# Performance work log

Hardware: AMD Instinct MI355X
Metric: run time of the kernel (lower is better)

Reference implementation:

```python
import jax, jax.numpy as jnp
import numpy as np

N_NODES = 100000
N_EDGES = 1600000
MSG = 16
HID = 16
N_ETYPE = 8
N_CLASSES = 40


def setup_inputs() -> dict:
    key = jax.random.key(0)
    ks = jax.random.split(key, 11)
    return {
        "features": jax.random.normal(ks[0], (N_NODES, HID), dtype=jnp.float32),
        "src": jax.random.randint(ks[1], (N_EDGES,), 0, N_NODES),
        "dst": jax.random.randint(ks[2], (N_EDGES,), 0, N_NODES),
        "etype": jax.random.randint(ks[3], (N_EDGES,), 0, N_ETYPE),
        "edge_matrix": jax.random.normal(ks[4], (N_ETYPE, MSG * HID), dtype=jnp.float32) * 0.1,
        "w_ih": jax.random.normal(ks[5], (3 * HID, MSG), dtype=jnp.float32) * 0.1,
        "w_hh": jax.random.normal(ks[6], (3 * HID, HID), dtype=jnp.float32) * 0.1,
        "b_ih": jax.random.normal(ks[7], (3 * HID,), dtype=jnp.float32) * 0.1,
        "b_hh": jax.random.normal(ks[8], (3 * HID,), dtype=jnp.float32) * 0.1,
        "out_w": jax.random.normal(ks[9], (N_CLASSES, HID), dtype=jnp.float32) * 0.1,
        "out_b": jax.random.normal(ks[10], (N_CLASSES,), dtype=jnp.float32) * 0.1,
    }


def reference(features, src, dst, etype, edge_matrix, w_ih, w_hh, b_ih, b_hh, out_w, out_b):
    n = features.shape[0]
    # message: per-edge [MSG,HID] matrix (gathered by edge type) times src h
    A = edge_matrix[etype].reshape(-1, MSG, HID)          # [E, MSG, HID]
    msg = jnp.einsum('emh,eh->em', A, features[src])      # [E, MSG]
    # reduce: scatter-sum messages onto destination nodes
    m = jax.ops.segment_sum(msg, dst, num_segments=n)     # [N, MSG]
    # apply: one GRU step per node (PyTorch nn.GRU gate math)
    gi = m @ w_ih.T + b_ih                                # [N, 3*HID]
    gh = features @ w_hh.T + b_hh                         # [N, 3*HID]
    i_r, i_z, i_n = jnp.split(gi, 3, axis=-1)
    h_r, h_z, h_n = jnp.split(gh, 3, axis=-1)
    r = jax.nn.sigmoid(i_r + h_r)
    z = jax.nn.sigmoid(i_z + h_z)
    c = jnp.tanh(i_n + r * h_n)
    h = (1.0 - z) * c + z * features                      # [N, HID]
    return h @ out_w.T + out_b                            # [N, N_CLASSES]
```

## Files before the change

### kernel.cpp

```cpp
#include <hip/hip_runtime.h>
#include <math.h>

constexpr int N_NODES   = 100000;
constexpr int N_EDGES   = 1600000;
constexpr int MSG       = 16;
constexpr int HID       = 16;
constexpr int N_ETYPE   = 8;
constexpr int N_CLASSES = 40;

constexpr int CBSIZE   = 256;
constexpr int NBUCKET  = (N_NODES + CBSIZE - 1) / CBSIZE;
constexpr int SBSIZE   = 32;
constexpr int NSUB     = 8;
constexpr int NSB      = NBUCKET * NSUB;
constexpr int EPB      = 4096;
constexpr int NEBLK    = (N_EDGES + EPB - 1) / EPB;
constexpr int REC_CAP  = 5120;
constexpr int FGRID    = 1536;
constexpr int NSLOT    = 2048;
constexpr int A_STRIDE = 260;
constexpr int SRECC    = 1792;

__device__ __forceinline__ float sigmoidf_(float x) { return 1.0f / (1.0f + __expf(-x)); }
__device__ __forceinline__ float tanhf_(float x) { float e = __expf(2.0f * x); return 1.0f - 2.0f / (e + 1.0f); }

__device__ __forceinline__ unsigned f2bf(float f) {
    unsigned u = __float_as_uint(f);
    return (u + 0x7FFFu + ((u >> 16) & 1u)) >> 16;
}
__device__ __forceinline__ float bflo(unsigned u) { return __uint_as_float(u << 16); }
__device__ __forceinline__ float bfhi(unsigned u) { return __uint_as_float(u & 0xFFFF0000u); }

__global__ void __launch_bounds__(256) cvt_kernel(const float* __restrict__ features,
                                                  uint4* __restrict__ featb,
                                                  int* __restrict__ gcursor) {
    int i = blockIdx.x * 256 + threadIdx.x;
    if (i < NBUCKET) gcursor[i] = i * REC_CAP;
    if (i * 8 >= N_NODES * HID) return;
    const float4* fp = reinterpret_cast<const float4*>(features + i * 8);
    float4 a = fp[0], b = fp[1];
    uint4 o;
    o.x = f2bf(a.x) | (f2bf(a.y) << 16);
    o.y = f2bf(a.z) | (f2bf(a.w) << 16);
    o.z = f2bf(b.x) | (f2bf(b.y) << 16);
    o.w = f2bf(b.z) | (f2bf(b.w) << 16);
    featb[i] = o;
}

__global__ void __launch_bounds__(512) partition_kernel(
    const int* __restrict__ src,
    const int* __restrict__ dst,
    const int* __restrict__ etype,
    int* __restrict__ gcursor,
    int* __restrict__ records)
{
    __shared__ int srec[EPB];
    __shared__ unsigned short sbkt[EPB];
    __shared__ int lh[NBUCKET];
    __shared__ int lscan[NBUCKET];
    __shared__ int gbarr[NBUCKET];
    __shared__ int wsum[8];

    int t = threadIdx.x;
    int base = blockIdx.x * EPB;

    for (int i = t; i < NBUCKET; i += 512) lh[i] = 0;
    __syncthreads();

    int rr[8]; int bb[8]; int rk[8];
    #pragma unroll
    for (int q = 0; q < 8; ++q) {
        int e = base + t + 512 * q;
        if (e < N_EDGES) {
            int d = dst[e];
            bb[q] = d >> 8;
            rr[q] = (src[e] << 11) | (etype[e] << 8) | (d & 255);
            rk[q] = atomicAdd(&lh[bb[q]], 1);
        } else bb[q] = -1;
    }
    __syncthreads();

    int i0 = t * 4;
    int v0 = 0, v1 = 0, v2 = 0, v3 = 0;
    if (i0     < NBUCKET) v0 = lh[i0];
    if (i0 + 1 < NBUCKET) v1 = lh[i0 + 1];
    if (i0 + 2 < NBUCKET) v2 = lh[i0 + 2];
    if (i0 + 3 < NBUCKET) v3 = lh[i0 + 3];
    int tsum = v0 + v1 + v2 + v3;

    int lane = t & 63, w = t >> 6;
    int inc = tsum;
    #pragma unroll
    for (int off = 1; off < 64; off <<= 1) {
        int u = __shfl_up(inc, off, 64);
        if (lane >= off) inc += u;
    }
    if (lane == 63) wsum[w] = inc;
    __syncthreads();
    int basew = 0;
    #pragma unroll
    for (int i = 0; i < 8; ++i) if (i < w) basew += wsum[i];
    int excl = basew + inc - tsum;

    if (i0     < NBUCKET) { lscan[i0]     = excl; gbarr[i0]     = v0 ? atomicAdd(&gcursor[i0],     v0) : 0; } excl += v0;
    if (i0 + 1 < NBUCKET) { lscan[i0 + 1] = excl; gbarr[i0 + 1] = v1 ? atomicAdd(&gcursor[i0 + 1], v1) : 0; } excl += v1;
    if (i0 + 2 < NBUCKET) { lscan[i0 + 2] = excl; gbarr[i0 + 2] = v2 ? atomicAdd(&gcursor[i0 + 2], v2) : 0; } excl += v2;
    if (i0 + 3 < NBUCKET) { lscan[i0 + 3] = excl; gbarr[i0 + 3] = v3 ? atomicAdd(&gcursor[i0 + 3], v3) : 0; }
    __syncthreads();

    #pragma unroll
    for (int q = 0; q < 8; ++q) {
        if (bb[q] >= 0) {
            int sidx = lscan[bb[q]] + rk[q];
            srec[sidx] = rr[q];
            sbkt[sidx] = (unsigned short)bb[q];
        }
    }
    __syncthreads();

    int cnt = min(EPB, N_EDGES - base);
    for (int s2 = t; s2 < cnt; s2 += 512) {
        int b2 = sbkt[s2];
        int pos = gbarr[b2] + (s2 - lscan[b2]);
        if (pos < (b2 + 1) * REC_CAP)
            records[pos] = srec[s2];
    }
}

__global__ void __launch_bounds__(256) partition2_kernel(
    const int* __restrict__ gcursor,
    const int* __restrict__ records,
    int* __restrict__ records2,
    int* __restrict__ slot_off)
{
    __shared__ int hist[NSLOT];
    __shared__ int wsum[4];
    __shared__ int srec[REC_CAP];

    int cb = blockIdx.x;
    int beg = cb * REC_CAP;
    int cnt = min(gcursor[cb] - beg, REC_CAP);
    int t = threadIdx.x;

    #pragma unroll
    for (int j = 0; j < 8; ++j) hist[t * 8 + j] = 0;
    __syncthreads();

    for (int i = t; i < cnt; i += 256) {
        int r = records[beg + i];
        atomicAdd(&hist[((r & 255) << 3) | ((r >> 8) & 7)], 1);
    }
    __syncthreads();

    int loc[8]; int tsum = 0;
    #pragma unroll
    for (int j = 0; j < 8; ++j) { loc[j] = hist[t * 8 + j]; tsum += loc[j]; }

    int lane = t & 63, w = t >> 6;
    int inc = tsum;
    #pragma unroll
    for (int off = 1; off < 64; off <<= 1) {
        int u = __shfl_up(inc, off, 64);
        if (lane >= off) inc += u;
    }
    if (lane == 63) wsum[w] = inc;
    __syncthreads();
    int basew = 0;
    #pragma unroll
    for (int i = 0; i < 4; ++i) if (i < w) basew += wsum[i];
    int excl = basew + inc - tsum;

    #pragma unroll
    for (int j = 0; j < 8; ++j) {
        slot_off[cb * (NSLOT + 1) + t * 8 + j] = beg + excl;
        hist[t * 8 + j] = excl;
        excl += loc[j];
    }
    if (t == 0) slot_off[cb * (NSLOT + 1) + NSLOT] = beg + cnt;
    __syncthreads();

    for (int i = t; i < cnt; i += 256) {
        int r = records[beg + i];
        int pos = atomicAdd(&hist[((r & 255) << 3) | ((r >> 8) & 7)], 1);
        srec[pos] = r;
    }
    __syncthreads();
    for (int i = t; i < cnt; i += 256) records2[beg + i] = srec[i];
}

__global__ void __launch_bounds__(256, 6) fused_kernel(
    const uint4* __restrict__ featb,
    const float* __restrict__ features,
    const int*   __restrict__ slot_off,
    const int*   __restrict__ records2,
    const float* __restrict__ edge_matrix,
    const float* __restrict__ w_ih,
    const float* __restrict__ w_hh,
    const float* __restrict__ b_ih,
    const float* __restrict__ b_hh,
    const float* __restrict__ out_w,
    const float* __restrict__ out_b,
    float*       __restrict__ out)
{
    __shared__ float A[N_ETYPE * A_STRIDE];
    __shared__ float wihL[3 * HID * 17];
    __shared__ float whhL[3 * HID * 17];
    __shared__ float outwL[N_CLASSES * 17];
    __shared__ float bihL[3 * HID];
    __shared__ float bhhL[3 * HID];
    __shared__ float outbL[N_CLASSES];
    __shared__ int   srecL[SRECC];

    int t = threadIdx.x;
    int dl = t >> 3, q = t & 7;
    const float4* feat4 = reinterpret_cast<const float4*>(features);

    for (int i = t; i < N_ETYPE * MSG * HID; i += 256)
        A[(i >> 8) * A_STRIDE + (i & 255)] = edge_matrix[i];
    for (int i = t; i < 3 * HID * MSG; i += 256) wihL[(i >> 4) * 17 + (i & 15)] = w_ih[i];
    for (int i = t; i < 3 * HID * HID; i += 256) whhL[(i >> 4) * 17 + (i & 15)] = w_hh[i];
    for (int i = t; i < N_CLASSES * HID; i += 256) outwL[(i >> 4) * 17 + (i & 15)] = out_w[i];
    if (t < 48) bihL[t] = b_ih[t];
    else if (t < 96) bhhL[t - 48] = b_hh[t - 48];
    else if (t < 136) outbL[t - 96] = out_b[t - 96];

    for (int b = blockIdx.x; b < NSB; b += FGRID) {
        int nodeBase = b * SBSIZE;
        if (nodeBase >= N_NODES) continue;
        int cb = b >> 3, sb = b & 7;
        __syncthreads();

        int sobase = cb * (NSLOT + 1) + sb * 256;
        int S0 = slot_off[sobase];
        int S1 = slot_off[sobase + 256];
        int begin = slot_off[sobase + t];
        int end   = slot_off[sobase + t + 1];
        int lim = min(S1 - S0, SRECC);
        for (int i = t; i < lim; i += 256)
            srecL[i] = __builtin_nontemporal_load(records2 + S0 + i);
        __syncthreads();

        float acc[16];
        #pragma unroll
        for (int k = 0; k < 16; ++k) acc[k] = 0.0f;
        for (int i = begin; i < end; ++i) {
            int li = i - S0;
            int rec = (li < SRECC) ? srecL[li] : records2[i];
            int sn = rec >> 11;
            uint4 ua = featb[2 * sn], ub = featb[2 * sn + 1];
            acc[0]  += bflo(ua.x); acc[1]  += bfhi(ua.x);
            acc[2]  += bflo(ua.y); acc[3]  += bfhi(ua.y);
            acc[4]  += bflo(ua.z); acc[5]  += bfhi(ua.z);
            acc[6]  += bflo(ua.w); acc[7]  += bfhi(ua.w);
            acc[8]  += bflo(ub.x); acc[9]  += bfhi(ub.x);
            acc[10] += bflo(ub.y); acc[11] += bfhi(ub.y);
            acc[12] += bflo(ub.z); acc[13] += bfhi(ub.z);
            acc[14] += bflo(ub.w); acc[15] += bfhi(ub.w);
        }

        float p[16];
        {
            const float* Aq = &A[q * A_STRIDE];
            #pragma unroll
            for (int mm = 0; mm < 16; ++mm) {
                const float4* Ar = reinterpret_cast<const float4*>(Aq + mm * 16);
                float4 x0 = Ar[0], x1 = Ar[1], x2 = Ar[2], x3 = Ar[3];
                p[mm] = x0.x*acc[0]  + x0.y*acc[1]  + x0.z*acc[2]  + x0.w*acc[3]
                      + x1.x*acc[4]  + x1.y*acc[5]  + x1.z*acc[6]  + x1.w*acc[7]
                      + x2.x*acc[8]  + x2.y*acc[9]  + x2.z*acc[10] + x2.w*acc[11]
                      + x3.x*acc[12] + x3.y*acc[13] + x3.z*acc[14] + x3.w*acc[15];
            }
        }
        #pragma unroll
        for (int mm = 0; mm < 16; ++mm) {
            p[mm] += __shfl_xor(p[mm], 1, 64);
            p[mm] += __shfl_xor(p[mm], 2, 64);
            p[mm] += __shfl_xor(p[mm], 4, 64);
        }

        int n = nodeBase + dl;
        float hva[16];
        {
            const float4* hp = feat4 + (size_t)n * 4;
            float4 h0 = hp[0], h1 = hp[1], h2 = hp[2], h3 = hp[3];
            hva[0]=h0.x; hva[1]=h0.y; hva[2]=h0.z; hva[3]=h0.w;
            hva[4]=h1.x; hva[5]=h1.y; hva[6]=h1.z; hva[7]=h1.w;
            hva[8]=h2.x; hva[9]=h2.y; hva[10]=h2.z; hva[11]=h2.w;
            hva[12]=h3.x; hva[13]=h3.y; hva[14]=h3.z; hva[15]=h3.w;
        }
        float hg[2];
        #pragma unroll
        for (int jj = 0; jj < 2; ++jj) {
            int j = 2 * q + jj;
            float ir  = bihL[j];
            float iz  = bihL[j + HID];
            float inn = bihL[j + 2 * HID];
            float hr  = bhhL[j];
            float hz  = bhhL[j + HID];
            float hnn = bhhL[j + 2 * HID];
            const float* wir = &wihL[j * 17];
            const float* wiz = &wihL[(j + HID) * 17];
            const float* win = &wihL[(j + 2 * HID) * 17];
            const float* whr = &whhL[j * 17];
            const float* whz = &whhL[(j + HID) * 17];
            const float* whn = &whhL[(j + 2 * HID) * 17];
            #pragma unroll
            for (int k = 0; k < HID; ++k) {
                ir  += wir[k] * p[k];
                iz  += wiz[k] * p[k];
                inn += win[k] * p[k];
                hr  += whr[k] * hva[k];
                hz  += whz[k] * hva[k];
                hnn += whn[k] * hva[k];
            }
            float rg = sigmoidf_(ir + hr);
            float zg = sigmoidf_(iz + hz);
            float cg = tanhf_(inn + rg * hnn);
            float hj = features[(size_t)n * HID + j];
            hg[jj] = (1.0f - zg) * cg + zg * hj;
        }

        int lanebase = (t & 63) & 56;
        float hh[16];
        #pragma unroll
        for (int qq = 0; qq < 8; ++qq) {
            hh[2 * qq]     = __shfl(hg[0], lanebase + qq, 64);
            hh[2 * qq + 1] = __shfl(hg[1], lanebase + qq, 64);
        }

        float* op = out + (size_t)n * N_CLASSES + 5 * q;
        #pragma unroll
        for (int cc = 0; cc < 5; ++cc) {
            int c = 5 * q + cc;
            float a2 = outbL[c];
            const float* wr = &outwL[c * 17];
            #pragma unroll
            for (int k = 0; k < HID; ++k) a2 += wr[k] * hh[k];
            __builtin_nontemporal_store(a2, op + cc);
        }
    }
}

extern "C" void kernel_launch(void* const* d_in, const int* in_sizes, int n_in,
                              void* d_out, int out_size, void* d_ws, size_t ws_size,
                              hipStream_t stream) {
    const float* features    = (const float*)d_in[0];
    const int*   src         = (const int*)  d_in[1];
    const int*   dst         = (const int*)  d_in[2];
    const int*   etype       = (const int*)  d_in[3];
    const float* edge_matrix = (const float*)d_in[4];
    const float* w_ih        = (const float*)d_in[5];
    const float* w_hh        = (const float*)d_in[6];
    const float* b_ih        = (const float*)d_in[7];
    const float* b_hh        = (const float*)d_in[8];
    const float* out_w       = (const float*)d_in[9];
    const float* out_b       = (const float*)d_in[10];
    float* out = (float*)d_out;

    int* gcursor  = (int*)d_ws;
    int* slot_off = gcursor + NBUCKET;
    int* records  = slot_off + NBUCKET * (NSLOT + 1);
    int* records2 = records + NBUCKET * REC_CAP;
    size_t featb_off = ((size_t)((char*)(records2 + NBUCKET * REC_CAP) - (char*)d_ws) + 15) & ~15ull;
    uint4* featb = (uint4*)((char*)d_ws + featb_off);

    cvt_kernel<<<(N_NODES * HID / 8 + 255) / 256, 256, 0, stream>>>(features, featb, gcursor);
    partition_kernel<<<NEBLK, 512, 0, stream>>>(src, dst, etype, gcursor, records);
    partition2_kernel<<<NBUCKET, 256, 0, stream>>>(gcursor, records, records2, slot_off);
    fused_kernel<<<FGRID, 256, 0, stream>>>(
        featb, features, slot_off, records2, edge_matrix,
        w_ih, w_hh, b_ih, b_hh, out_w, out_b, out);
}
```

Measured before the change: 119.6 us.

## Use atomic work-stealing for sub-buckets and stage outputs through shared memory

The fused kernel stops striding sub-buckets statically and instead hands them out dynamically through a global atomic counter, which is initialised in the conversion kernel. This is meant to balance blocks when edge counts per sub-bucket vary. Hidden states now go through a shared transposed buffer, and the 40-class outputs are staged in shared memory so they can be written as coalesced float4 nontemporal stores. The shared record cache is shrunk and reused as the output staging area, which adds barriers and an atomic per iteration.

```diff
diff --git a/kernel.cpp b/kernel.cpp
--- a/kernel.cpp
+++ b/kernel.cpp
@@ -19,7 +19,9 @@
 constexpr int FGRID    = 1536;
 constexpr int NSLOT    = 2048;
 constexpr int A_STRIDE = 260;
-constexpr int SRECC    = 1792;
+constexpr int SRECC    = 1536;
+
+typedef float vfloat4 __attribute__((ext_vector_type(4)));
 
 __device__ __forceinline__ float sigmoidf_(float x) { return 1.0f / (1.0f + __expf(-x)); }
 __device__ __forceinline__ float tanhf_(float x) { float e = __expf(2.0f * x); return 1.0f - 2.0f / (e + 1.0f); }
@@ -36,6 +38,7 @@
                                                   int* __restrict__ gcursor) {
     int i = blockIdx.x * 256 + threadIdx.x;
     if (i < NBUCKET) gcursor[i] = i * REC_CAP;
+    else if (i == NBUCKET) gcursor[i] = FGRID;
     if (i * 8 >= N_NODES * HID) return;
     const float4* fp = reinterpret_cast<const float4*>(features + i * 8);
     float4 a = fp[0], b = fp[1];
@@ -193,6 +196,7 @@
     const float* __restrict__ features,
     const int*   __restrict__ slot_off,
     const int*   __restrict__ records2,
+    int*         __restrict__ wcnt,
     const float* __restrict__ edge_matrix,
     const float* __restrict__ w_ih,
     const float* __restrict__ w_hh,
@@ -209,11 +213,18 @@
     __shared__ float bihL[3 * HID];
     __shared__ float bhhL[3 * HID];
     __shared__ float outbL[N_CLASSES];
-    __shared__ int   srecL[SRECC];
+    __shared__ float hnT[HID][SBSIZE + 1];
+    __shared__ int   uni[SRECC];
+    __shared__ int   bS;
+
+    int* srecL = uni;
+    float* outS = reinterpret_cast<float*>(uni);
 
     int t = threadIdx.x;
     int dl = t >> 3, q = t & 7;
     const float4* feat4 = reinterpret_cast<const float4*>(features);
+
+    if (t == 0) bS = blockIdx.x;
 
     for (int i = t; i < N_ETYPE * MSG * HID; i += 256)
         A[(i >> 8) * A_STRIDE + (i & 255)] = edge_matrix[i];
@@ -223,121 +234,141 @@
     if (t < 48) bihL[t] = b_ih[t];
     else if (t < 96) bhhL[t - 48] = b_hh[t - 48];
     else if (t < 136) outbL[t - 96] = out_b[t - 96];
-
-    for (int b = blockIdx.x; b < NSB; b += FGRID) {
+    __syncthreads();
+
+    for (;;) {
+        int b = bS;
+        if (b >= NSB) break;
         int nodeBase = b * SBSIZE;
-        if (nodeBase >= N_NODES) continue;
+        bool active = nodeBase < N_NODES;
         int cb = b >> 3, sb = b & 7;
+
+        int S0 = 0, begin = 0, end = 0;
+        if (active) {
+            int sobase = cb * (NSLOT + 1) + sb * 256;
+            S0 = slot_off[sobase];
+            int S1 = slot_off[sobase + 256];
+            begin = slot_off[sobase + t];
+            end   = slot_off[sobase + t + 1];
+            int lim = min(S1 - S0, SRECC);
+            for (int i = t; i < lim; i += 256)
+                srecL[i] = __builtin_nontemporal_load(records2 + S0 + i);
+        }
         __syncthreads();
 
-        int sobase = cb * (NSLOT + 1) + sb * 256;
-        int S0 = slot_off[sobase];
-        int S1 = slot_off[sobase + 256];
-        int begin = slot_off[sobase + t];
-        int end   = slot_off[sobase + t + 1];
-        int lim = min(S1 - S0, SRECC);
-        for (int i = t; i < lim; i += 256)
-            srecL[i] = __builtin_nontemporal_load(records2 + S0 + i);
+        if (t == 0) bS = atomicAdd(wcnt, 1);
+
+        if (active) {
+            float acc[16];
+            #pragma unroll
+            for (int k = 0; k < 16; ++k) acc[k] = 0.0f;
+            for (int i = begin; i < end; ++i) {
+                int li = i - S0;
+                int rec = (li < SRECC) ? srecL[li] : records2[i];
+                int sn = rec >> 11;
+                uint4 ua = featb[2 * sn], ub = featb[2 * sn + 1];
+                acc[0]  += bflo(ua.x); acc[1]  += bfhi(ua.x);
+                acc[2]  += bflo(ua.y); acc[3]  += bfhi(ua.y);
+                acc[4]  += bflo(ua.z); acc[5]  += bfhi(ua.z);
+                acc[6]  += bflo(ua.w); acc[7]  += bfhi(ua.w);
+                acc[8]  += bflo(ub.x); acc[9]  += bfhi(ub.x);
+                acc[10] += bflo(ub.y); acc[11] += bfhi(ub.y);
+                acc[12] += bflo(ub.z); acc[13] += bfhi(ub.z);
+                acc[14] += bflo(ub.w); acc[15] += bfhi(ub.w);
+            }
+
+            float p[16];
+            {
+                const float* Aq = &A[q * A_STRIDE];
+                #pragma unroll
+                for (int mm = 0; mm < 16; ++mm) {
+                    const float4* Ar = reinterpret_cast<const float4*>(Aq + mm * 16);
+                    float4 x0 = Ar[0], x1 = Ar[1], x2 = Ar[2], x3 = Ar[3];
+                    p[mm] = x0.x*acc[0]  + x0.y*acc[1]  + x0.z*acc[2]  + x0.w*acc[3]
+                          + x1.x*acc[4]  + x1.y*acc[5]  + x1.z*acc[6]  + x1.w*acc[7]
+                          + x2.x*acc[8]  + x2.y*acc[9]  + x2.z*acc[10] + x2.w*acc[11]
+                          + x3.x*acc[12] + x3.y*acc[13] + x3.z*acc[14] + x3.w*acc[15];
+                }
+            }
+            #pragma unroll
+            for (int mm = 0; mm < 16; ++mm) {
+                p[mm] += __shfl_xor(p[mm], 1, 64);
+                p[mm] += __shfl_xor(p[mm], 2, 64);
+                p[mm] += __shfl_xor(p[mm], 4, 64);
+            }
+
+            int n = nodeBase + dl;
+            float hva[16];
+            {
+                const float4* hp = feat4 + (size_t)n * 4;
+                float4 h0 = hp[0], h1 = hp[1], h2 = hp[2], h3 = hp[3];
+                hva[0]=h0.x; hva[1]=h0.y; hva[2]=h0.z; hva[3]=h0.w;
+                hva[4]=h1.x; hva[5]=h1.y; hva[6]=h1.z; hva[7]=h1.w;
+                hva[8]=h2.x; hva[9]=h2.y; hva[10]=h2.z; hva[11]=h2.w;
+                hva[12]=h3.x; hva[13]=h3.y; hva[14]=h3.z; hva[15]=h3.w;
+            }
+            #pragma unroll
+            for (int jj = 0; jj < 2; ++jj) {
+                int j = 2 * q + jj;
+                float ir  = bihL[j];
+                float iz  = bihL[j + HID];
+                float inn = bihL[j + 2 * HID];
+                float hr  = bhhL[j];
+                float hz  = bhhL[j + HID];
+                float hnn = bhhL[j + 2 * HID];
+                const float* wir = &wihL[j * 17];
+                const float* wiz = &wihL[(j + HID) * 17];
+                const float* win = &wihL[(j + 2 * HID) * 17];
+                const float* whr = &whhL[j * 17];
+                const float* whz = &whhL[(j + HID) * 17];
+                const float* whn = &whhL[(j + 2 * HID) * 17];
+                #pragma unroll
+                for (int k = 0; k < HID; ++k) {
+                    ir  += wir[k] * p[k];
+                    iz  += wiz[k] * p[k];
+                    inn += win[k] * p[k];
+                    hr  += whr[k] * hva[k];
+                    hz  += whz[k] * hva[k];
+                    hnn += whn[k] * hva[k];
+                }
+                float rg = sigmoidf_(ir + hr);
+                float zg = sigmoidf_(iz + hz);
+                float cg = tanhf_(inn + rg * hnn);
+                float hj = features[(size_t)n * HID + j];
+                hnT[j][dl] = (1.0f - zg) * cg + zg * hj;
+            }
+        }
         __syncthreads();
 
-        float acc[16];
-        #pragma unroll
-        for (int k = 0; k < 16; ++k) acc[k] = 0.0f;
-        for (int i = begin; i < end; ++i) {
-            int li = i - S0;
-            int rec = (li < SRECC) ? srecL[li] : records2[i];
-            int sn = rec >> 11;
-            uint4 ua = featb[2 * sn], ub = featb[2 * sn + 1];
-            acc[0]  += bflo(ua.x); acc[1]  += bfhi(ua.x);
-            acc[2]  += bflo(ua.y); acc[3]  += bfhi(ua.y);
-            acc[4]  += bflo(ua.z); acc[5]  += bfhi(ua.z);
-            acc[6]  += bflo(ua.w); acc[7]  += bfhi(ua.w);
-            acc[8]  += bflo(ub.x); acc[9]  += bfhi(ub.x);
-            acc[10] += bflo(ub.y); acc[11] += bfhi(ub.y);
-            acc[12] += bflo(ub.z); acc[13] += bfhi(ub.z);
-            acc[14] += bflo(ub.w); acc[15] += bfhi(ub.w);
+        if (active) {
+            float hh[HID];
+            #pragma unroll
+            for (int k = 0; k < HID; ++k) hh[k] = hnT[k][dl];
+            #pragma unroll
+            for (int cc = 0; cc < 5; ++cc) {
+                int c = 5 * q + cc;
+                float a2 = outbL[c];
+                const float* wr = &outwL[c * 17];
+                #pragma unroll
+                for (int k = 0; k < HID; ++k) a2 += wr[k] * hh[k];
+                outS[dl * 44 + c] = a2;
+            }
         }
-
-        float p[16];
-        {
-            const float* Aq = &A[q * A_STRIDE];
-            #pragma unroll
-            for (int mm = 0; mm < 16; ++mm) {
-                const float4* Ar = reinterpret_cast<const float4*>(Aq + mm * 16);
-                float4 x0 = Ar[0], x1 = Ar[1], x2 = Ar[2], x3 = Ar[3];
-                p[mm] = x0.x*acc[0]  + x0.y*acc[1]  + x0.z*acc[2]  + x0.w*acc[3]
-                      + x1.x*acc[4]  + x1.y*acc[5]  + x1.z*acc[6]  + x1.w*acc[7]
-                      + x2.x*acc[8]  + x2.y*acc[9]  + x2.z*acc[10] + x2.w*acc[11]
-                      + x3.x*acc[12] + x3.y*acc[13] + x3.z*acc[14] + x3.w*acc[15];
+        __syncthreads();
+
+        if (active) {
+            vfloat4* ob4 = reinterpret_cast<vfloat4*>(out + (size_t)nodeBase * N_CLASSES);
+            #pragma unroll
+            for (int rep = 0; rep < 2; ++rep) {
+                int i = t + rep * 256;
+                if (i < SBSIZE * N_CLASSES / 4) {
+                    int node = i / 10, qq = i - node * 10;
+                    vfloat4 v = *reinterpret_cast<const vfloat4*>(&outS[node * 44 + qq * 4]);
+                    __builtin_nontemporal_store(v, ob4 + i);
+                }
             }
         }
-        #pragma unroll
-        for (int mm = 0; mm < 16; ++mm) {
-            p[mm] += __shfl_xor(p[mm], 1, 64);
-            p[mm] += __shfl_xor(p[mm], 2, 64);
-            p[mm] += __shfl_xor(p[mm], 4, 64);
-        }
-
-        int n = nodeBase + dl;
-        float hva[16];
-        {
-            const float4* hp = feat4 + (size_t)n * 4;
-            float4 h0 = hp[0], h1 = hp[1], h2 = hp[2], h3 = hp[3];
-            hva[0]=h0.x; hva[1]=h0.y; hva[2]=h0.z; hva[3]=h0.w;
-            hva[4]=h1.x; hva[5]=h1.y; hva[6]=h1.z; hva[7]=h1.w;
-            hva[8]=h2.x; hva[9]=h2.y; hva[10]=h2.z; hva[11]=h2.w;
-            hva[12]=h3.x; hva[13]=h3.y; hva[14]=h3.z; hva[15]=h3.w;
-        }
-        float hg[2];
-        #pragma unroll
-        for (int jj = 0; jj < 2; ++jj) {
-            int j = 2 * q + jj;
-            float ir  = bihL[j];
-            float iz  = bihL[j + HID];
-            float inn = bihL[j + 2 * HID];
-            float hr  = bhhL[j];
-            float hz  = bhhL[j + HID];
-            float hnn = bhhL[j + 2 * HID];
-            const float* wir = &wihL[j * 17];
-            const float* wiz = &wihL[(j + HID) * 17];
-            const float* win = &wihL[(j + 2 * HID) * 17];
-            const float* whr = &whhL[j * 17];
-            const float* whz = &whhL[(j + HID) * 17];
-            const float* whn = &whhL[(j + 2 * HID) * 17];
-            #pragma unroll
-            for (int k = 0; k < HID; ++k) {
-                ir  += wir[k] * p[k];
-                iz  += wiz[k] * p[k];
-                inn += win[k] * p[k];
-                hr  += whr[k] * hva[k];
-                hz  += whz[k] * hva[k];
-                hnn += whn[k] * hva[k];
-            }
-            float rg = sigmoidf_(ir + hr);
-            float zg = sigmoidf_(iz + hz);
-            float cg = tanhf_(inn + rg * hnn);
-            float hj = features[(size_t)n * HID + j];
-            hg[jj] = (1.0f - zg) * cg + zg * hj;
-        }
-
-        int lanebase = (t & 63) & 56;
-        float hh[16];
-        #pragma unroll
-        for (int qq = 0; qq < 8; ++qq) {
-            hh[2 * qq]     = __shfl(hg[0], lanebase + qq, 64);
-            hh[2 * qq + 1] = __shfl(hg[1], lanebase + qq, 64);
-        }
-
-        float* op = out + (size_t)n * N_CLASSES + 5 * q;
-        #pragma unroll
-        for (int cc = 0; cc < 5; ++cc) {
-            int c = 5 * q + cc;
-            float a2 = outbL[c];
-            const float* wr = &outwL[c * 17];
-            #pragma unroll
-            for (int k = 0; k < HID; ++k) a2 += wr[k] * hh[k];
-            __builtin_nontemporal_store(a2, op + cc);
-        }
+        __syncthreads();
     }
 }
 
@@ -358,7 +389,8 @@
     float* out = (float*)d_out;
 
     int* gcursor  = (int*)d_ws;
-    int* slot_off = gcursor + NBUCKET;
+    int* wcnt     = gcursor + NBUCKET;
+    int* slot_off = wcnt + 1;
     int* records  = slot_off + NBUCKET * (NSLOT + 1);
     int* records2 = records + NBUCKET * REC_CAP;
     size_t featb_off = ((size_t)((char*)(records2 + NBUCKET * REC_CAP) - (char*)d_ws) + 15) & ~15ull;
@@ -368,6 +400,6 @@
     partition_kernel<<<NEBLK, 512, 0, stream>>>(src, dst, etype, gcursor, records);
     partition2_kernel<<<NBUCKET, 256, 0, stream>>>(gcursor, records, records2, slot_off);
     fused_kernel<<<FGRID, 256, 0, stream>>>(
-        featb, features, slot_off, records2, edge_matrix,
+        featb, features, slot_off, records2, wcnt, edge_matrix,
         w_ih, w_hh, b_ih, b_hh, out_w, out_b, out);
 }
```

Result: no change. 121.0 us (+1.2%).
